# Performance work log

Measured on AMD Instinct MI355X. Metric: run time of the kernel, lower is better.

The kernel has to match this reference:

```python
import jax, jax.numpy as jnp
import numpy as np

HID = 768
NSPLITS = 12
HEAD_RATIO = 2
H = NSPLITS // HEAD_RATIO          # 6 attention heads
D = HID // NSPLITS                 # 64 head size
AH = H * D                         # 384 all_head_size
KS = 9                             # conv kernel size
PAD = (KS - 1) // 2
B, S = 4, 1024


def setup_inputs() -> dict:
    key = jax.random.key(0)
    ks = jax.random.split(key, 16)
    std = 0.02
    inp = {
        "Q": jax.random.normal(ks[0], (B, S, HID), jnp.float32),
        "K": jax.random.normal(ks[1], (B, S, HID), jnp.float32),
        "V": jax.random.normal(ks[2], (B, S, HID), jnp.float32),
        "td": jax.random.uniform(ks[3], (B, S), jnp.float32),
        "mask": jax.random.randint(ks[4], (B, S), 0, 2, jnp.int32),
        # projection weights, applied as x @ W (in, out)
        "Wq": jax.random.normal(ks[5], (HID, AH), jnp.float32) * std,
        "Wk": jax.random.normal(ks[6], (HID, AH), jnp.float32) * std,
        "Wv": jax.random.normal(ks[7], (HID, AH), jnp.float32) * std,
        # separable conv: depthwise (HID, KS), pointwise (AH, HID), bias (AH,)
        "dw_w": jax.random.normal(ks[8], (HID, KS), jnp.float32) * std,
        "pw_w": jax.random.normal(ks[9], (AH, HID), jnp.float32) * std,
        "sep_b": jnp.zeros((AH,), jnp.float32),
        # conv_kernel_layer Linear(AH -> H*KS)
        "ck_W": jax.random.normal(ks[10], (AH, H * KS), jnp.float32) * std,
        "ck_b": jnp.zeros((H * KS,), jnp.float32),
        # conv_out_layer Linear(HID -> AH)
        "co_W": jax.random.normal(ks[11], (HID, AH), jnp.float32) * std,
        "co_b": jnp.zeros((AH,), jnp.float32),
        # gammas init to zeros as in torch module
        "gammas": jnp.zeros((H, 1, 1), jnp.float32),
    }
    return inp


def dist_func(scores, td, am, gammas):
    # scores: [B,H,S,S]; am: [B,1,1,S] bool key mask; entirely non-differentiable.
    s = scores.shape[-1]
    dt = scores.dtype
    amf = am.astype(dt)
    p = jax.nn.softmax(jnp.where(am, scores, -1e8), axis=-1) * amf
    distcum = jnp.cumsum(p, axis=-1)
    disttotal = jnp.sum(p, axis=-1, keepdims=True)
    # |j - i| position distance
    pos = jnp.abs(jnp.arange(s)[None, :] - jnp.arange(s)[:, None]).astype(dt)
    dist_scores = jnp.sqrt(jnp.clip((disttotal - distcum) * pos[None, None], 0.0, None))
    gamma = -jax.nn.softplus(gammas)[None]  # (1,H,1,1)
    total_effect = jnp.clip(jnp.exp(dist_scores * gamma), 1e-5, 1e5)
    # time-distance effect on strictly-lower-triangular positions
    tdn = td / jnp.maximum(jnp.linalg.norm(td, axis=-1, keepdims=True), 1e-12)
    td_scores = jnp.broadcast_to(tdn[:, None, None, :], scores.shape)
    td_sm = jax.nn.softmax(jnp.where(am, td_scores, -1e4), axis=-1)
    lower = jnp.tril(jnp.ones((s, s), dt), -1)  # (triu == 0)
    return jax.lax.stop_gradient(total_effect - td_sm * lower[None, None])


def reference(Q, K, V, td, mask, Wq, Wk, Wv, dw_w, pw_w, sep_b, ck_W, ck_b, co_W, co_b, gammas):
    b, s, hid = Q.shape
    mq = Q @ Wq  # (B,S,AH)
    mk = K @ Wk
    mv = V @ Wv
    # SeparableConv1D over sequence dim of K
    x = jnp.transpose(K, (0, 2, 1))  # (B,HID,S)
    dw = jax.lax.conv_general_dilated(
        x, dw_w[:, None, :], window_strides=(1,), padding=[(PAD, PAD)],
        feature_group_count=hid, dimension_numbers=("NCH", "OIH", "NCH"))
    pw = jnp.einsum("bcs,oc->bos", dw, pw_w) + sep_b[None, :, None]
    mkc = jnp.transpose(pw, (0, 2, 1))  # (B,S,AH)

    q = mq.reshape(b, s, H, D).transpose(0, 2, 1, 3)
    k = mk.reshape(b, s, H, D).transpose(0, 2, 1, 3)
    v = mv.reshape(b, s, H, D).transpose(0, 2, 1, 3)

    # dynamic span convolution
    conv_attn = mkc * mq                                   # (B,S,AH)
    ck = (conv_attn @ ck_W + ck_b).reshape(b, s, H, KS)
    ck = jax.nn.softmax(ck, axis=-1)                       # per-position kernel
    co = V @ co_W + co_b                                   # (B,S,AH)
    co_pad = jnp.pad(co, ((0, 0), (PAD, PAD), (0, 0)))
    idx = jnp.arange(s)[:, None] + jnp.arange(KS)[None, :]  # (S,KS)
    unf = co_pad[:, idx, :].reshape(b, s, KS, H, D)         # sliding window gather
    conv_out = jnp.einsum("bskhd,bshk->bshd", unf, ck)      # (B,S,H,D)

    # attention with distance decay
    scores = jnp.einsum("bhid,bhjd->bhij", q, k) / np.float32(np.sqrt(D))
    am = (mask[:, None, None, :] != 0)  # (B,1,1,S) key mask
    total_effect = dist_func(scores, td, am, gammas)
    scores = jnp.where(am, scores * total_effect, -1e8)
    probs = jax.nn.softmax(scores, axis=-1)
    ctx = jnp.einsum("bhij,bhjd->bhid", probs, v).transpose(0, 2, 1, 3)  # (B,S,H,D)

    out = jnp.concatenate([ctx, conv_out], axis=2).reshape(b, s, HEAD_RATIO * AH)
    return out
```

## Files before the change

kernel.cpp:

```cpp
#include <hip/hip_runtime.h>
#include <hip/hip_bf16.h>

#define HIDC 768
#define Hh   6
#define Dd   64
#define AHc  384
#define KSc  9
#define PADc 4
#define Bb   4
#define Ss   1024
#define MRr  (Bb * Ss)

typedef __attribute__((ext_vector_type(8))) __bf16 bf16x8;
typedef __attribute__((ext_vector_type(4))) __bf16 bf16x4;
typedef __attribute__((ext_vector_type(4))) float  f32x4;

__device__ __forceinline__ void gl_lds16(const void* g, void* l) {
    __builtin_amdgcn_global_load_lds(
        (const __attribute__((address_space(1))) void*)g,
        (__attribute__((address_space(3))) void*)l, 16, 0, 0);
}

__device__ __forceinline__ void split8(const float* p, bf16x8& hi, bf16x8& lo) {
    float4 x0 = *(const float4*)p;
    float4 x1 = *(const float4*)(p + 4);
    float xs[8] = {x0.x, x0.y, x0.z, x0.w, x1.x, x1.y, x1.z, x1.w};
#pragma unroll
    for (int e = 0; e < 8; ++e) {
        __bf16 hv = (__bf16)xs[e];
        hi[e] = hv;
        lo[e] = (__bf16)(xs[e] - (float)hv);
    }
}

__device__ __forceinline__ void split8r(const float* xs, bf16x8& hi, bf16x8& lo) {
#pragma unroll
    for (int e = 0; e < 8; ++e) {
        __bf16 hv = (__bf16)xs[e];
        hi[e] = hv;
        lo[e] = (__bf16)(xs[e] - (float)hv);
    }
}

__device__ __forceinline__ bf16x8 cvt8(const float* p) {
    float4 x0 = *(const float4*)p;
    float4 x1 = *(const float4*)(p + 4);
    float xs[8] = {x0.x, x0.y, x0.z, x0.w, x1.x, x1.y, x1.z, x1.w};
    bf16x8 h;
#pragma unroll
    for (int e = 0; e < 8; ++e) h[e] = (__bf16)xs[e];
    return h;
}

__global__ void k_dwab(const float* __restrict__ Kin, const float* __restrict__ dww,
                       const float* __restrict__ Q, const float* __restrict__ V,
                       __bf16* __restrict__ dwbf,
                       __bf16* __restrict__ qbf, __bf16* __restrict__ vbf) {
    int bid = blockIdx.x;
    if (bid < 3072) {
        int idx = bid * 256 + threadIdx.x;
        int c4 = idx % (HIDC / 4);
        int s  = (idx / (HIDC / 4)) % Ss;
        int b  = idx / ((HIDC / 4) * Ss);
        int c  = c4 * 4;
        float wv[4][KSc];
#pragma unroll
        for (int j = 0; j < 4; ++j)
#pragma unroll
            for (int k = 0; k < KSc; ++k) wv[j][k] = dww[(c + j) * KSc + k];
        float4 acc = {0.f, 0.f, 0.f, 0.f};
#pragma unroll
        for (int k = 0; k < KSc; ++k) {
            int sp = s + k - PADc;
            if (sp >= 0 && sp < Ss) {
                float4 v = *(const float4*)&Kin[(size_t)(b * Ss + sp) * HIDC + c];
                acc.x += v.x * wv[0][k]; acc.y += v.y * wv[1][k];
                acc.z += v.z * wv[2][k]; acc.w += v.w * wv[3][k];
            }
        }
        bf16x4 o = {(__bf16)acc.x, (__bf16)acc.y, (__bf16)acc.z, (__bf16)acc.w};
        *(bf16x4*)(dwbf + (size_t)idx * 4) = o;
    } else {
        const int n8 = MRr * HIDC / 8;
        int idx = (bid - 3072) * 256 + threadIdx.x;
        if (idx < n8) {
            *(bf16x8*)(qbf + (size_t)idx * 8) = cvt8(Q + (size_t)idx * 8);
        } else {
            int i = idx - n8;
            *(bf16x8*)(vbf + (size_t)i * 8) = cvt8(V + (size_t)i * 8);
        }
    }
}

__global__ __launch_bounds__(256) void k_wsplit_t(const float* __restrict__ Wq, const float* __restrict__ Wk,
                                                  const float* __restrict__ Wv, const float* __restrict__ coW,
                                                  __bf16* __restrict__ Whi, __bf16* __restrict__ Wlo) {
    int z = blockIdx.z;
    const float* src = (z == 0) ? Wq : (z == 1) ? Wk : (z == 2) ? Wv : coW;
    int n0 = blockIdx.x * 64, k0 = blockIdx.y * 64;
    int tid = threadIdx.x;
    int r = tid >> 2, cq = tid & 3;
    __shared__ float tile[64][65];
#pragma unroll
    for (int e = 0; e < 4; ++e) {
        float4 v = *(const float4*)&src[(size_t)(k0 + r) * AHc + n0 + cq * 16 + e * 4];
        tile[r][cq * 16 + e * 4 + 0] = v.x;
        tile[r][cq * 16 + e * 4 + 1] = v.y;
        tile[r][cq * 16 + e * 4 + 2] = v.z;
        tile[r][cq * 16 + e * 4 + 3] = v.w;
    }
    __syncthreads();
    float x[16];
#pragma unroll
    for (int e = 0; e < 16; ++e) x[e] = tile[cq * 16 + e][r];
    bf16x8 h0, l0, h1, l1;
    split8r(x, h0, l0);
    split8r(x + 8, h1, l1);
    size_t dst = ((size_t)(z * AHc + n0 + r)) * HIDC + k0 + cq * 16;
    *(bf16x8*)(Whi + dst)     = h0;
    *(bf16x8*)(Whi + dst + 8) = h1;
    *(bf16x8*)(Wlo + dst)     = l0;
    *(bf16x8*)(Wlo + dst + 8) = l1;
}

__global__ __launch_bounds__(256) void k_misc(const float* __restrict__ pww,
                                              const float* __restrict__ cob, const float* __restrict__ sepb,
                                              const float* __restrict__ td, const int* __restrict__ mask,
                                              __bf16* __restrict__ Whi, __bf16* __restrict__ Wlo,
                                              float* __restrict__ biasb, float* __restrict__ td_sm) {
    int bid = blockIdx.x;
    int tid = threadIdx.x;
    if (bid < 144) {
        int idx = bid * 256 + tid;
        bf16x8 hi, lo;
        split8(pww + (size_t)idx * 8, hi, lo);
        size_t dst = (size_t)4 * AHc * HIDC + (size_t)idx * 8;
        *(bf16x8*)(Whi + dst) = hi;
        *(bf16x8*)(Wlo + dst) = lo;
        return;
    }
    if (bid < 152) {
        int idx = (bid - 144) * 256 + tid;
        if (idx < 5 * AHc) {
            int z = idx / AHc, n = idx % AHc;
            biasb[idx] = (z == 3) ? cob[n] : (z == 4) ? sepb[n] : 0.f;
        }
        return;
    }
    int b = bid - 152;
    __shared__ float red[256];
    __shared__ float tv[Ss];
    float ls = 0.f;
    for (int j = tid; j < Ss; j += 256) {
        float v = td[b * Ss + j];
        tv[j] = v;
        ls += v * v;
    }
    red[tid] = ls; __syncthreads();
    for (int s = 128; s > 0; s >>= 1) { if (tid < s) red[tid] += red[tid + s]; __syncthreads(); }
    float norm = fmaxf(sqrtf(red[0]), 1e-12f);
    __syncthreads();
    float lm = -3e38f;
    for (int j = tid; j < Ss; j += 256) {
        float v = mask[b * Ss + j] ? tv[j] / norm : -1e4f;
        tv[j] = v;
        lm = fmaxf(lm, v);
    }
    red[tid] = lm; __syncthreads();
    for (int s = 128; s > 0; s >>= 1) { if (tid < s) red[tid] = fmaxf(red[tid], red[tid + s]); __syncthreads(); }
    float m = red[0]; __syncthreads();
    float lsum = 0.f;
    for (int j = tid; j < Ss; j += 256) {
        float e = expf(tv[j] - m);
        tv[j] = e;
        lsum += e;
    }
    red[tid] = lsum; __syncthreads();
    for (int s = 128; s > 0; s >>= 1) { if (tid < s) red[tid] += red[tid + s]; __syncthreads(); }
    float inv = 1.f / red[0];
    __syncthreads();
    for (int j = tid; j < Ss; j += 256)
        td_sm[b * Ss + j] = tv[j] * inv;
}

__global__ __launch_bounds__(256) void k_gemm5(
        const __bf16* __restrict__ qbf, const float* __restrict__ Kin,
        const __bf16* __restrict__ vbf, const __bf16* __restrict__ dwbf,
        const __bf16* __restrict__ Whi, const __bf16* __restrict__ Wlo,
        const float* __restrict__ biasb, float* __restrict__ Call,
        __bf16* __restrict__ kh, __bf16* __restrict__ kl,
        __bf16* __restrict__ qh, __bf16* __restrict__ vt) {
    __shared__ __attribute__((aligned(16))) __bf16 As [128 * 32];
    __shared__ __attribute__((aligned(16))) __bf16 BsH[128 * 32];
    __shared__ __attribute__((aligned(16))) __bf16 BsL[128 * 32];

    int wg = blockIdx.x + 3 * (blockIdx.y + 32 * blockIdx.z);
    int n2 = (wg & 7) * 60 + (wg >> 3);
    int bxx = n2 % 3, byy = (n2 / 3) % 32, z = n2 / 96;

    int m0 = byy * 128, n0 = bxx * 128;
    int tid = threadIdx.x;
    int wave = tid >> 6, lane = tid & 63, quad = lane >> 4, l15 = lane & 15;

    int lrow = lane >> 2;
    int lswz = 8 * ((lane & 3) ^ (lrow & 3));

    int brow = wave * 32 + lrow;
    const __bf16* BhG0 = Whi + ((size_t)(z * AHc + n0 + brow)) * HIDC + lswz;
    const __bf16* BhG1 = BhG0 + (size_t)16 * HIDC;
    const __bf16* BlG0 = Wlo + ((size_t)(z * AHc + n0 + brow)) * HIDC + lswz;
    const __bf16* BlG1 = BlG0 + (size_t)16 * HIDC;
    __bf16* BhL0 = BsH + (wave * 2 + 0) * 512;
    __bf16* BhL1 = BsH + (wave * 2 + 1) * 512;
    __bf16* BlL0 = BsL + (wave * 2 + 0) * 512;
    __bf16* BlL1 = BsL + (wave * 2 + 1) * 512;

    const __bf16* Abf = (z == 0) ? qbf : (z == 4) ? dwbf : vbf;
    const __bf16* AG0 = Abf + ((size_t)(m0 + wave * 32 + lrow)) * HIDC + lswz;
    const __bf16* AG1 = AG0 + (size_t)16 * HIDC;
    __bf16* AL0 = As + (wave * 2 + 0) * 512;
    __bf16* AL1 = As + (wave * 2 + 1) * 512;

    int sr = tid >> 1;
    int sk = (tid & 1) * 16;
    const float* Arow = Kin + (size_t)(m0 + sr) * HIDC + sk;
    int g0 = sk >> 3;
    int d0 = sr * 32 + ((g0       ^ (sr & 3)) * 8);
    int d1 = sr * 32 + (((g0 + 1) ^ (sr & 3)) * 8);

    int swz = (quad ^ (l15 & 3)) * 8;
    f32x4 acc[4][4] = {};

    for (int k0 = 0; k0 < HIDC; k0 += 32) {
        if (z == 1) {
            const float* ap = Arow + k0;
            *(bf16x8*)&As[d0] = cvt8(ap);
            *(bf16x8*)&As[d1] = cvt8(ap + 8);
        } else {
            gl_lds16(AG0 + k0, AL0);
            gl_lds16(AG1 + k0, AL1);
        }
        gl_lds16(BhG0 + k0, BhL0);
        gl_lds16(BhG1 + k0, BhL1);
        gl_lds16(BlG0 + k0, BlL0);
        gl_lds16(BlG1 + k0, BlL1);
        __syncthreads();

        int mrow = (wave >> 1) * 64 + l15;
        int nrow = (wave & 1) * 64 + l15;
        bf16x8 ah[4], bh[4], bl[4];
#pragma unroll
        for (int mt = 0; mt < 4; ++mt)
            ah[mt] = *(bf16x8*)&As[(mrow + mt * 16) * 32 + swz];
#pragma unroll
        for (int nt = 0; nt < 4; ++nt) {
            bh[nt] = *(bf16x8*)&BsH[(nrow + nt * 16) * 32 + swz];
            bl[nt] = *(bf16x8*)&BsL[(nrow + nt * 16) * 32 + swz];
        }
#pragma unroll
        for (int mt = 0; mt < 4; ++mt)
#pragma unroll
            for (int nt = 0; nt < 4; ++nt) {
                acc[mt][nt] = __builtin_amdgcn_mfma_f32_16x16x32_bf16(ah[mt], bh[nt], acc[mt][nt], 0, 0, 0);
                acc[mt][nt] = __builtin_amdgcn_mfma_f32_16x16x32_bf16(ah[mt], bl[nt], acc[mt][nt], 0, 0, 0);
            }
        __syncthreads();
    }

    if (z == 1) {
#pragma unroll
        for (int nt = 0; nt < 4; ++nt) {
            int n = n0 + (wave & 1) * 64 + nt * 16 + l15;
#pragma unroll
            for (int mt = 0; mt < 4; ++mt) {
#pragma unroll
                for (int r = 0; r < 4; ++r) {
                    int m = m0 + (wave >> 1) * 64 + mt * 16 + quad * 4 + r;
                    float v = acc[mt][nt][r];
                    __bf16 hv = (__bf16)v;
                    kh[(size_t)m * AHc + n] = hv;
                    kl[(size_t)m * AHc + n] = (__bf16)(v - (float)hv);
                }
            }
        }
    } else if (z == 2) {
        int b = m0 >> 10;
#pragma unroll
        for (int nt = 0; nt < 4; ++nt) {
            int n = (wave & 1) * 64 + nt * 16 + l15;
            int gn = n0 + n;
            int h = gn >> 6, d = gn & 63;
#pragma unroll
            for (int mt = 0; mt < 4; ++mt) {
                int m = m0 + (wave >> 1) * 64 + mt * 16 + quad * 4;
                int s = m & (Ss - 1);
                bf16x4 o = {(__bf16)acc[mt][nt][0], (__bf16)acc[mt][nt][1],
                            (__bf16)acc[mt][nt][2], (__bf16)acc[mt][nt][3]};
                *(bf16x4*)&vt[((size_t)((b * Hh + h) * Dd + d)) * Ss + s] = o;
            }
        }
    } else if (z == 0) {
#pragma unroll
        for (int nt = 0; nt < 4; ++nt) {
            int n = n0 + (wave & 1) * 64 + nt * 16 + l15;
#pragma unroll
            for (int mt = 0; mt < 4; ++mt) {
#pragma unroll
                for (int r = 0; r < 4; ++r) {
                    int m = m0 + (wave >> 1) * 64 + mt * 16 + quad * 4 + r;
                    float v = acc[mt][nt][r];
                    Call[(size_t)m * AHc + n] = v;
                    qh[(size_t)m * AHc + n] = (__bf16)v;
                }
            }
        }
    } else {
        float* Cz = Call + (size_t)z * MRr * AHc;
        const float* bz = biasb + z * AHc;
#pragma unroll
        for (int nt = 0; nt < 4; ++nt) {
            int n = n0 + (wave & 1) * 64 + nt * 16 + l15;
            float bias = bz[n];
#pragma unroll
            for (int mt = 0; mt < 4; ++mt) {
#pragma unroll
                for (int r = 0; r < 4; ++r) {
                    int m = m0 + (wave >> 1) * 64 + mt * 16 + quad * 4 + r;
                    Cz[(size_t)m * AHc + n] = acc[mt][nt][r] + bias;
                }
            }
        }
    }
}

__global__ __launch_bounds__(64) void k_ck(const float* __restrict__ mkc, const float* __restrict__ mq,
                                           const float* __restrict__ ckW, const float* __restrict__ ckb,
                                           float* __restrict__ ck_sm) {
    int row = blockIdx.x;
    int tid = threadIdx.x;
    __shared__ float ca[AHc];
    __shared__ float ckv[Hh * KSc];
    for (int o = tid; o < AHc; o += 64)
        ca[o] = mkc[row * AHc + o] * mq[row * AHc + o];
    __syncthreads();
    if (tid < Hh * KSc) {
        float acc = ckb[tid];
        for (int o = 0; o < AHc; ++o)
            acc += ca[o] * ckW[o * (Hh * KSc) + tid];
        ckv[tid] = acc;
    }
    __syncthreads();
    if (tid < Hh) {
        float m = -3e38f;
#pragma unroll
        for (int k = 0; k < KSc; ++k) m = fmaxf(m, ckv[tid * KSc + k]);
        float e[KSc];
        float s = 0.f;
#pragma unroll
        for (int k = 0; k < KSc; ++k) { e[k] = expf(ckv[tid * KSc + k] - m); s += e[k]; }
        float inv = 1.f / s;
#pragma unroll
        for (int k = 0; k < KSc; ++k) ck_sm[(row * Hh + tid) * KSc + k] = e[k] * inv;
    }
}

__global__ void k_convout(const float* __restrict__ co, const float* __restrict__ ck_sm,
                          float* __restrict__ out) {
    int idx = blockIdx.x * 256 + threadIdx.x;
    if (idx >= Bb * Ss * AHc / 4) return;
    int d4 = idx & 15;
    int h  = (idx >> 4) % Hh;
    int s  = (idx / (AHc / 4)) % Ss;
    int b  = idx / ((AHc / 4) * Ss);
    int row = b * Ss + s;
    const float* ck = ck_sm + (size_t)(row * Hh + h) * KSc;
    float4 acc = {0.f, 0.f, 0.f, 0.f};
#pragma unroll
    for (int k = 0; k < KSc; ++k) {
        int sp = s + k - PADc;
        if (sp >= 0 && sp < Ss) {
            float4 v = *(const float4*)&co[(size_t)(b * Ss + sp) * AHc + h * Dd + d4 * 4];
            float wv = ck[k];
            acc.x += wv * v.x; acc.y += wv * v.y; acc.z += wv * v.z; acc.w += wv * v.w;
        }
    }
    *(float4*)&out[(size_t)row * (2 * AHc) + AHc + h * Dd + d4 * 4] = acc;
}

__device__ __forceinline__ int scix(int m, int j) {
    return m * 1024 + (j ^ (((m ^ (j >> 6)) & 7) << 2));
}

__global__ __launch_bounds__(512) void k_attn(const __bf16* __restrict__ qh,
                                              const __bf16* __restrict__ kh, const __bf16* __restrict__ kl,
                                              const __bf16* __restrict__ vt,
                                              const int* __restrict__ mask,
                                              const float* __restrict__ td_sm, const float* __restrict__ gammas,
                                              float* __restrict__ out) {
    __shared__ float sc[16 * 1024];
    int wg = blockIdx.x + 64 * blockIdx.y;
    int n  = (wg & 7) * 192 + (wg >> 3);
    int bx = n & 63, by = n >> 6;
    int i0 = bx * 16;
    int h = by % Hh, b = by / Hh;
    int tid = threadIdx.x;
    int w = tid >> 6, lane = tid & 63, quad = lane >> 4, l15 = lane & 15;
    int jw = w * 128;

    bf16x8 a_hi[2];
    {
        size_t qoff = (size_t)(b * Ss + i0 + l15) * AHc + h * Dd + quad * 8;
        a_hi[0] = *(const bf16x8*)(qh + qoff);
        a_hi[1] = *(const bf16x8*)(qh + qoff + 32);
    }
#pragma unroll 2
    for (int t = 0; t < 8; ++t) {
        int jt = jw + t * 16;
        size_t koff = (size_t)(b * Ss + jt + l15) * AHc + h * Dd + quad * 8;
        f32x4 acc = {0.f, 0.f, 0.f, 0.f};
#pragma unroll
        for (int kc = 0; kc < 2; ++kc) {
            bf16x8 khv = *(const bf16x8*)(kh + koff + kc * 32);
            bf16x8 klv = *(const bf16x8*)(kl + koff + kc * 32);
            acc = __builtin_amdgcn_mfma_f32_16x16x32_bf16(a_hi[kc], khv, acc, 0, 0, 0);
            acc = __builtin_amdgcn_mfma_f32_16x16x32_bf16(a_hi[kc], klv, acc, 0, 0, 0);
        }
#pragma unroll
        for (int r = 0; r < 4; ++r)
            sc[scix(quad * 4 + r, jt + l15)] = acc[r] * 0.125f;
    }
    __syncthreads();

    const int* mrow = mask + b * Ss;
    const float* tdrow = td_sm + b * Ss;
    float gamma = -log1pf(expf(gammas[h]));
    int jb = lane << 4;
    __attribute__((aligned(16))) int marr[16];
    {
        const int4* mp = (const int4*)(mrow + jb);
#pragma unroll
        for (int k = 0; k < 4; ++k) ((int4*)marr)[k] = mp[k];
    }
    __attribute__((aligned(16))) float tdv[16];
    {
        const float4* tp = (const float4*)(tdrow + jb);
#pragma unroll
        for (int k = 0; k < 4; ++k) ((float4*)tdv)[k] = tp[k];
    }

#pragma unroll
    for (int r4 = 0; r4 < 2; ++r4) {
        int m = w * 2 + r4;
        int i = i0 + m;
        __attribute__((aligned(16))) float s[16];
        float p[16];
#pragma unroll
        for (int g = 0; g < 4; ++g)
            *(f32x4*)(s + 4 * g) = *(const f32x4*)&sc[scix(m, jb + 4 * g)];
        float mx = -1e30f;
#pragma unroll
        for (int jj = 0; jj < 16; ++jj) mx = fmaxf(mx, marr[jj] ? s[jj] : -1e30f);
        mx = fmaxf(mx, __shfl_xor(mx, 1));  mx = fmaxf(mx, __shfl_xor(mx, 2));
        mx = fmaxf(mx, __shfl_xor(mx, 4));  mx = fmaxf(mx, __shfl_xor(mx, 8));
        mx = fmaxf(mx, __shfl_xor(mx, 16)); mx = fmaxf(mx, __shfl_xor(mx, 32));
#pragma unroll
        for (int jj = 0; jj < 16; ++jj) p[jj] = marr[jj] ? __expf(s[jj] - mx) : 0.f;
#pragma unroll
        for (int jj = 1; jj < 16; ++jj) p[jj] += p[jj - 1];
        float t = p[15];
        float incl = t;
#pragma unroll
        for (int dlt = 1; dlt < 64; dlt <<= 1) {
            float v = __shfl_up(incl, dlt);
            if (lane >= dlt) incl += v;
        }
        float off = incl - t;
        float tot = __shfl(incl, 63);
        float inv = 1.f / fmaxf(tot, 1e-30f);
        float mx2 = -1e30f;
#pragma unroll
        for (int jj = 0; jj < 16; ++jj) {
            int j = jb + jj;
            float cum = p[jj] + off;
            float pos = fabsf((float)(j - i));
            float ds = sqrtf(fmaxf((tot - cum) * inv * pos, 0.f));
            float te = fminf(fmaxf(__expf(ds * gamma), 1e-5f), 1e5f);
            float mult = te - ((j < i) ? tdv[jj] : 0.f);
            float s2 = marr[jj] ? s[jj] * mult : -1e8f;
            s[jj] = s2;
            mx2 = fmaxf(mx2, s2);
        }
        mx2 = fmaxf(mx2, __shfl_xor(mx2, 1));  mx2 = fmaxf(mx2, __shfl_xor(mx2, 2));
        mx2 = fmaxf(mx2, __shfl_xor(mx2, 4));  mx2 = fmaxf(mx2, __shfl_xor(mx2, 8));
        mx2 = fmaxf(mx2, __shfl_xor(mx2, 16)); mx2 = fmaxf(mx2, __shfl_xor(mx2, 32));
        float sm = 0.f;
#pragma unroll
        for (int jj = 0; jj < 16; ++jj) { s[jj] = __expf(s[jj] - mx2); sm += s[jj]; }
        sm += __shfl_xor(sm, 1);  sm += __shfl_xor(sm, 2);
        sm += __shfl_xor(sm, 4);  sm += __shfl_xor(sm, 8);
        sm += __shfl_xor(sm, 16); sm += __shfl_xor(sm, 32);
        float inv2 = 1.f / sm;
#pragma unroll
        for (int jj = 0; jj < 16; ++jj) s[jj] *= inv2;
#pragma unroll
        for (int g = 0; g < 4; ++g)
            *(f32x4*)&sc[scix(m, jb + 4 * g)] = *(const f32x4*)(s + 4 * g);
    }
    __syncthreads();

    f32x4 oacc[4] = {};
    const __bf16* vtb = vt + (size_t)(b * Hh + h) * Dd * Ss;
#pragma unroll
    for (int kc = 0; kc < 4; ++kc) {
        int j0 = jw + kc * 32 + quad * 8;
        __attribute__((aligned(16))) float x[8];
        *(f32x4*)x       = *(const f32x4*)&sc[scix(l15, j0)];
        *(f32x4*)(x + 4) = *(const f32x4*)&sc[scix(l15, j0 + 4)];
        bf16x8 p_hi, p_lo;
        split8r(x, p_hi, p_lo);
#pragma unroll
        for (int nt = 0; nt < 4; ++nt) {
            int d = nt * 16 + l15;
            bf16x8 vv = *(const bf16x8*)(vtb + (size_t)d * Ss + j0);
            oacc[nt] = __builtin_amdgcn_mfma_f32_16x16x32_bf16(p_hi, vv, oacc[nt], 0, 0, 0);
            oacc[nt] = __builtin_amdgcn_mfma_f32_16x16x32_bf16(p_lo, vv, oacc[nt], 0, 0, 0);
        }
    }
    __syncthreads();
#pragma unroll
    for (int nt = 0; nt < 4; ++nt)
#pragma unroll
        for (int r = 0; r < 4; ++r)
            sc[w * 1024 + (quad * 4 + r) * 64 + nt * 16 + l15] = oacc[nt][r];
    __syncthreads();
#pragma unroll
    for (int e = 0; e < 2; ++e) {
        int idx = e * 512 + tid;
        int m = idx >> 6, dd = idx & 63;
        float v = 0.f;
#pragma unroll
        for (int ww = 0; ww < 8; ++ww) v += sc[ww * 1024 + idx];
        out[(size_t)(b * Ss + i0 + m) * (2 * AHc) + h * Dd + dd] = v;
    }
}

extern "C" void kernel_launch(void* const* d_in, const int* in_sizes, int n_in,
                              void* d_out, int out_size, void* d_ws, size_t ws_size,
                              hipStream_t stream) {
    const float* Q    = (const float*)d_in[0];
    const float* Kin  = (const float*)d_in[1];
    const float* V    = (const float*)d_in[2];
    const float* td   = (const float*)d_in[3];
    const int*   mask = (const int*)d_in[4];
    const float* Wq   = (const float*)d_in[5];
    const float* Wk   = (const float*)d_in[6];
    const float* Wv   = (const float*)d_in[7];
    const float* dww  = (const float*)d_in[8];
    const float* pww  = (const float*)d_in[9];
    const float* sepb = (const float*)d_in[10];
    const float* ckW  = (const float*)d_in[11];
    const float* ckb  = (const float*)d_in[12];
    const float* coW  = (const float*)d_in[13];
    const float* cob  = (const float*)d_in[14];
    const float* gam  = (const float*)d_in[15];
    float* out = (float*)d_out;
    float* ws = (float*)d_ws;

    float* mq    = ws;
    float* mks   = mq    + (size_t)MRr * AHc;
    float* mvs   = mks   + (size_t)MRr * AHc;
    float* co    = mvs   + (size_t)MRr * AHc;
    float* mkc   = co    + (size_t)MRr * AHc;
    float* dwr   = mkc   + (size_t)MRr * AHc;
    float* cksm  = dwr   + (size_t)MRr * HIDC;
    float* tdsm  = cksm  + (size_t)MRr * Hh * KSc;
    float* biasb = tdsm  + (size_t)Bb * Ss;

    __bf16* dwbf = (__bf16*)dwr;
    __bf16* qbf  = (__bf16*)(dwr + (size_t)MRr * HIDC / 2);
    __bf16* kh = (__bf16*)mks;
    __bf16* kl = kh + (size_t)MRr * AHc;
    __bf16* vt = (__bf16*)mvs;
    __bf16* qh = vt + (size_t)MRr * AHc;

    __bf16* Whi = (__bf16*)d_out;
    __bf16* Wlo = Whi + (size_t)5 * AHc * HIDC;
    __bf16* vbf = Wlo + (size_t)5 * AHc * HIDC;

    dim3 gt(AHc / 64, HIDC / 64, 4);
    k_wsplit_t<<<gt, 256, 0, stream>>>(Wq, Wk, Wv, coW, Whi, Wlo);
    k_misc<<<156, 256, 0, stream>>>(pww, cob, sepb, td, mask, Whi, Wlo, biasb, tdsm);
    k_dwab<<<6144, 256, 0, stream>>>(Kin, dww, Q, V, dwbf, qbf, vbf);

    dim3 gg(AHc / 128, MRr / 128, 5);
    k_gemm5<<<gg, 256, 0, stream>>>(qbf, Kin, vbf, dwbf, Whi, Wlo, biasb, mq, kh, kl, qh, vt);

    k_ck<<<MRr, 64, 0, stream>>>(mkc, mq, ckW, ckb, cksm);
    k_convout<<<(MRr * AHc / 4 + 255) / 256, 256, 0, stream>>>(co, cksm, out);

    dim3 ga(Ss / 16, Bb * Hh);
    k_attn<<<ga, 512, 0, stream>>>(qh, kh, kl, vt, mask, tdsm, gam, out);
}
```

Measured before the change: 281.7 us.

## Merge preprocessing kernels, fuse ck softmax with conv-out, interleave attention row pairs

Three preprocessing kernels (weight split/transpose, misc bias/td softmax, depthwise conv plus bf16 casts) are merged into one launch. The per-row kernel-weight softmax and the dynamic conv output are fused into one kernel that handles 4 rows per block, dropping the intermediate ck buffer and one launch. In attention, the two per-wave rows of the distance-decay softmax are processed interleaved for more ILP, the QK loop unroll is raised, and a min-blocks launch bound is added. Register pressure from the interleaving and the occupancy hint could cause spills.

```diff
diff --git a/kernel.cpp b/kernel.cpp
--- a/kernel.cpp
+++ b/kernel.cpp
@@ -52,13 +52,106 @@
     return h;
 }
 
-__global__ void k_dwab(const float* __restrict__ Kin, const float* __restrict__ dww,
-                       const float* __restrict__ Q, const float* __restrict__ V,
-                       __bf16* __restrict__ dwbf,
-                       __bf16* __restrict__ qbf, __bf16* __restrict__ vbf) {
+__global__ __launch_bounds__(256) void k_pre(
+        const float* __restrict__ Wq, const float* __restrict__ Wk,
+        const float* __restrict__ Wv, const float* __restrict__ coW,
+        const float* __restrict__ pww, const float* __restrict__ cob,
+        const float* __restrict__ sepb, const float* __restrict__ td,
+        const int* __restrict__ mask, const float* __restrict__ Kin,
+        const float* __restrict__ dww, const float* __restrict__ Q,
+        const float* __restrict__ V,
+        __bf16* __restrict__ Whi, __bf16* __restrict__ Wlo,
+        float* __restrict__ biasb, float* __restrict__ td_sm,
+        __bf16* __restrict__ dwbf, __bf16* __restrict__ qbf,
+        __bf16* __restrict__ vbf) {
+    __shared__ float shmem[64 * 65];
     int bid = blockIdx.x;
-    if (bid < 3072) {
-        int idx = bid * 256 + threadIdx.x;
+    int tid = threadIdx.x;
+    if (bid < 288) {
+        int z = bid / 72, rem = bid % 72;
+        int n0 = (rem % 6) * 64, k0 = (rem / 6) * 64;
+        const float* src = (z == 0) ? Wq : (z == 1) ? Wk : (z == 2) ? Wv : coW;
+        float (*tile)[65] = (float(*)[65])shmem;
+        int r = tid >> 2, cq = tid & 3;
+#pragma unroll
+        for (int e = 0; e < 4; ++e) {
+            float4 v = *(const float4*)&src[(size_t)(k0 + r) * AHc + n0 + cq * 16 + e * 4];
+            tile[r][cq * 16 + e * 4 + 0] = v.x;
+            tile[r][cq * 16 + e * 4 + 1] = v.y;
+            tile[r][cq * 16 + e * 4 + 2] = v.z;
+            tile[r][cq * 16 + e * 4 + 3] = v.w;
+        }
+        __syncthreads();
+        float x[16];
+#pragma unroll
+        for (int e = 0; e < 16; ++e) x[e] = tile[cq * 16 + e][r];
+        bf16x8 h0, l0, h1, l1;
+        split8r(x, h0, l0);
+        split8r(x + 8, h1, l1);
+        size_t dst = ((size_t)(z * AHc + n0 + r)) * HIDC + k0 + cq * 16;
+        *(bf16x8*)(Whi + dst)     = h0;
+        *(bf16x8*)(Whi + dst + 8) = h1;
+        *(bf16x8*)(Wlo + dst)     = l0;
+        *(bf16x8*)(Wlo + dst + 8) = l1;
+        return;
+    }
+    if (bid < 432) {
+        int idx = (bid - 288) * 256 + tid;
+        bf16x8 hi, lo;
+        split8(pww + (size_t)idx * 8, hi, lo);
+        size_t dst = (size_t)4 * AHc * HIDC + (size_t)idx * 8;
+        *(bf16x8*)(Whi + dst) = hi;
+        *(bf16x8*)(Wlo + dst) = lo;
+        return;
+    }
+    if (bid < 440) {
+        int idx = (bid - 432) * 256 + tid;
+        if (idx < 5 * AHc) {
+            int z = idx / AHc, n = idx % AHc;
+            biasb[idx] = (z == 3) ? cob[n] : (z == 4) ? sepb[n] : 0.f;
+        }
+        return;
+    }
+    if (bid < 444) {
+        int b = bid - 440;
+        float* red = shmem;
+        float* tv  = shmem + 256;
+        float ls = 0.f;
+        for (int j = tid; j < Ss; j += 256) {
+            float v = td[b * Ss + j];
+            tv[j] = v;
+            ls += v * v;
+        }
+        red[tid] = ls; __syncthreads();
+        for (int s = 128; s > 0; s >>= 1) { if (tid < s) red[tid] += red[tid + s]; __syncthreads(); }
+        float norm = fmaxf(sqrtf(red[0]), 1e-12f);
+        __syncthreads();
+        float lm = -3e38f;
+        for (int j = tid; j < Ss; j += 256) {
+            float v = mask[b * Ss + j] ? tv[j] / norm : -1e4f;
+            tv[j] = v;
+            lm = fmaxf(lm, v);
+        }
+        red[tid] = lm; __syncthreads();
+        for (int s = 128; s > 0; s >>= 1) { if (tid < s) red[tid] = fmaxf(red[tid], red[tid + s]); __syncthreads(); }
+        float m = red[0]; __syncthreads();
+        float lsum = 0.f;
+        for (int j = tid; j < Ss; j += 256) {
+            float e = expf(tv[j] - m);
+            tv[j] = e;
+            lsum += e;
+        }
+        red[tid] = lsum; __syncthreads();
+        for (int s = 128; s > 0; s >>= 1) { if (tid < s) red[tid] += red[tid + s]; __syncthreads(); }
+        float inv = 1.f / red[0];
+        __syncthreads();
+        for (int j = tid; j < Ss; j += 256)
+            td_sm[b * Ss + j] = tv[j] * inv;
+        return;
+    }
+    int db = bid - 444;
+    if (db < 3072) {
+        int idx = db * 256 + tid;
         int c4 = idx % (HIDC / 4);
         int s  = (idx / (HIDC / 4)) % Ss;
         int b  = idx / ((HIDC / 4) * Ss);
@@ -82,7 +175,7 @@
         *(bf16x4*)(dwbf + (size_t)idx * 4) = o;
     } else {
         const int n8 = MRr * HIDC / 8;
-        int idx = (bid - 3072) * 256 + threadIdx.x;
+        int idx = (db - 3072) * 256 + tid;
         if (idx < n8) {
             *(bf16x8*)(qbf + (size_t)idx * 8) = cvt8(Q + (size_t)idx * 8);
         } else {
@@ -90,97 +183,6 @@
             *(bf16x8*)(vbf + (size_t)i * 8) = cvt8(V + (size_t)i * 8);
         }
     }
-}
-
-__global__ __launch_bounds__(256) void k_wsplit_t(const float* __restrict__ Wq, const float* __restrict__ Wk,
-                                                  const float* __restrict__ Wv, const float* __restrict__ coW,
-                                                  __bf16* __restrict__ Whi, __bf16* __restrict__ Wlo) {
-    int z = blockIdx.z;
-    const float* src = (z == 0) ? Wq : (z == 1) ? Wk : (z == 2) ? Wv : coW;
-    int n0 = blockIdx.x * 64, k0 = blockIdx.y * 64;
-    int tid = threadIdx.x;
-    int r = tid >> 2, cq = tid & 3;
-    __shared__ float tile[64][65];
-#pragma unroll
-    for (int e = 0; e < 4; ++e) {
-        float4 v = *(const float4*)&src[(size_t)(k0 + r) * AHc + n0 + cq * 16 + e * 4];
-        tile[r][cq * 16 + e * 4 + 0] = v.x;
-        tile[r][cq * 16 + e * 4 + 1] = v.y;
-        tile[r][cq * 16 + e * 4 + 2] = v.z;
-        tile[r][cq * 16 + e * 4 + 3] = v.w;
-    }
-    __syncthreads();
-    float x[16];
-#pragma unroll
-    for (int e = 0; e < 16; ++e) x[e] = tile[cq * 16 + e][r];
-    bf16x8 h0, l0, h1, l1;
-    split8r(x, h0, l0);
-    split8r(x + 8, h1, l1);
-    size_t dst = ((size_t)(z * AHc + n0 + r)) * HIDC + k0 + cq * 16;
-    *(bf16x8*)(Whi + dst)     = h0;
-    *(bf16x8*)(Whi + dst + 8) = h1;
-    *(bf16x8*)(Wlo + dst)     = l0;
-    *(bf16x8*)(Wlo + dst + 8) = l1;
-}
-
-__global__ __launch_bounds__(256) void k_misc(const float* __restrict__ pww,
-                                              const float* __restrict__ cob, const float* __restrict__ sepb,
-                                              const float* __restrict__ td, const int* __restrict__ mask,
-                                              __bf16* __restrict__ Whi, __bf16* __restrict__ Wlo,
-                                              float* __restrict__ biasb, float* __restrict__ td_sm) {
-    int bid = blockIdx.x;
-    int tid = threadIdx.x;
-    if (bid < 144) {
-        int idx = bid * 256 + tid;
-        bf16x8 hi, lo;
-        split8(pww + (size_t)idx * 8, hi, lo);
-        size_t dst = (size_t)4 * AHc * HIDC + (size_t)idx * 8;
-        *(bf16x8*)(Whi + dst) = hi;
-        *(bf16x8*)(Wlo + dst) = lo;
-        return;
-    }
-    if (bid < 152) {
-        int idx = (bid - 144) * 256 + tid;
-        if (idx < 5 * AHc) {
-            int z = idx / AHc, n = idx % AHc;
-            biasb[idx] = (z == 3) ? cob[n] : (z == 4) ? sepb[n] : 0.f;
-        }
-        return;
-    }
-    int b = bid - 152;
-    __shared__ float red[256];
-    __shared__ float tv[Ss];
-    float ls = 0.f;
-    for (int j = tid; j < Ss; j += 256) {
-        float v = td[b * Ss + j];
-        tv[j] = v;
-        ls += v * v;
-    }
-    red[tid] = ls; __syncthreads();
-    for (int s = 128; s > 0; s >>= 1) { if (tid < s) red[tid] += red[tid + s]; __syncthreads(); }
-    float norm = fmaxf(sqrtf(red[0]), 1e-12f);
-    __syncthreads();
-    float lm = -3e38f;
-    for (int j = tid; j < Ss; j += 256) {
-        float v = mask[b * Ss + j] ? tv[j] / norm : -1e4f;
-        tv[j] = v;
-        lm = fmaxf(lm, v);
-    }
-    red[tid] = lm; __syncthreads();
-    for (int s = 128; s > 0; s >>= 1) { if (tid < s) red[tid] = fmaxf(red[tid], red[tid + s]); __syncthreads(); }
-    float m = red[0]; __syncthreads();
-    float lsum = 0.f;
-    for (int j = tid; j < Ss; j += 256) {
-        float e = expf(tv[j] - m);
-        tv[j] = e;
-        lsum += e;
-    }
-    red[tid] = lsum; __syncthreads();
-    for (int s = 128; s > 0; s >>= 1) { if (tid < s) red[tid] += red[tid + s]; __syncthreads(); }
-    float inv = 1.f / red[0];
-    __syncthreads();
-    for (int j = tid; j < Ss; j += 256)
-        td_sm[b * Ss + j] = tv[j] * inv;
 }
 
 __global__ __launch_bounds__(256) void k_gemm5(
@@ -333,65 +335,67 @@
     }
 }
 
-__global__ __launch_bounds__(64) void k_ck(const float* __restrict__ mkc, const float* __restrict__ mq,
-                                           const float* __restrict__ ckW, const float* __restrict__ ckb,
-                                           float* __restrict__ ck_sm) {
-    int row = blockIdx.x;
+__global__ __launch_bounds__(256) void k_ckconv(const float* __restrict__ mkc,
+                                                const float* __restrict__ mq,
+                                                const float* __restrict__ ckW,
+                                                const float* __restrict__ ckb,
+                                                const float* __restrict__ co,
+                                                float* __restrict__ out) {
     int tid = threadIdx.x;
-    __shared__ float ca[AHc];
-    __shared__ float ckv[Hh * KSc];
-    for (int o = tid; o < AHc; o += 64)
-        ca[o] = mkc[row * AHc + o] * mq[row * AHc + o];
+    int lr = tid >> 6, lane = tid & 63;
+    int row = blockIdx.x * 4 + lr;
+    __shared__ float ca[4][AHc];
+    __shared__ float ckv[4][Hh * KSc];
+    for (int o = lane; o < AHc; o += 64)
+        ca[lr][o] = mkc[(size_t)row * AHc + o] * mq[(size_t)row * AHc + o];
     __syncthreads();
-    if (tid < Hh * KSc) {
-        float acc = ckb[tid];
+    if (lane < Hh * KSc) {
+        float acc = ckb[lane];
         for (int o = 0; o < AHc; ++o)
-            acc += ca[o] * ckW[o * (Hh * KSc) + tid];
-        ckv[tid] = acc;
+            acc += ca[lr][o] * ckW[o * (Hh * KSc) + lane];
+        ckv[lr][lane] = acc;
     }
     __syncthreads();
-    if (tid < Hh) {
+    if (lane < Hh) {
         float m = -3e38f;
 #pragma unroll
-        for (int k = 0; k < KSc; ++k) m = fmaxf(m, ckv[tid * KSc + k]);
+        for (int k = 0; k < KSc; ++k) m = fmaxf(m, ckv[lr][lane * KSc + k]);
         float e[KSc];
         float s = 0.f;
 #pragma unroll
-        for (int k = 0; k < KSc; ++k) { e[k] = expf(ckv[tid * KSc + k] - m); s += e[k]; }
+        for (int k = 0; k < KSc; ++k) { e[k] = expf(ckv[lr][lane * KSc + k] - m); s += e[k]; }
         float inv = 1.f / s;
 #pragma unroll
-        for (int k = 0; k < KSc; ++k) ck_sm[(row * Hh + tid) * KSc + k] = e[k] * inv;
-    }
-}
-
-__global__ void k_convout(const float* __restrict__ co, const float* __restrict__ ck_sm,
-                          float* __restrict__ out) {
-    int idx = blockIdx.x * 256 + threadIdx.x;
-    if (idx >= Bb * Ss * AHc / 4) return;
-    int d4 = idx & 15;
-    int h  = (idx >> 4) % Hh;
-    int s  = (idx / (AHc / 4)) % Ss;
-    int b  = idx / ((AHc / 4) * Ss);
-    int row = b * Ss + s;
-    const float* ck = ck_sm + (size_t)(row * Hh + h) * KSc;
-    float4 acc = {0.f, 0.f, 0.f, 0.f};
-#pragma unroll
-    for (int k = 0; k < KSc; ++k) {
-        int sp = s + k - PADc;
-        if (sp >= 0 && sp < Ss) {
-            float4 v = *(const float4*)&co[(size_t)(b * Ss + sp) * AHc + h * Dd + d4 * 4];
-            float wv = ck[k];
-            acc.x += wv * v.x; acc.y += wv * v.y; acc.z += wv * v.z; acc.w += wv * v.w;
-        }
-    }
-    *(float4*)&out[(size_t)row * (2 * AHc) + AHc + h * Dd + d4 * 4] = acc;
+        for (int k = 0; k < KSc; ++k) ckv[lr][lane * KSc + k] = e[k] * inv;
+    }
+    __syncthreads();
+#pragma unroll
+    for (int e = 0; e < 2; ++e) {
+        int it = e * 256 + tid;
+        if (it >= 4 * (AHc / 4)) break;
+        int r4i = it / (AHc / 4), dq = it % (AHc / 4);
+        int h = dq >> 4, d4 = dq & 15;
+        int row2 = blockIdx.x * 4 + r4i;
+        int s = row2 & (Ss - 1), b = row2 >> 10;
+        float4 acc = {0.f, 0.f, 0.f, 0.f};
+#pragma unroll
+        for (int k = 0; k < KSc; ++k) {
+            int sp = s + k - PADc;
+            if (sp >= 0 && sp < Ss) {
+                float4 v = *(const float4*)&co[(size_t)(b * Ss + sp) * AHc + h * Dd + d4 * 4];
+                float wv = ckv[r4i][h * KSc + k];
+                acc.x += wv * v.x; acc.y += wv * v.y; acc.z += wv * v.z; acc.w += wv * v.w;
+            }
+        }
+        *(float4*)&out[(size_t)row2 * (2 * AHc) + AHc + h * Dd + d4 * 4] = acc;
+    }
 }
 
 __device__ __forceinline__ int scix(int m, int j) {
     return m * 1024 + (j ^ (((m ^ (j >> 6)) & 7) << 2));
 }
 
-__global__ __launch_bounds__(512) void k_attn(const __bf16* __restrict__ qh,
+__global__ __launch_bounds__(512, 4) void k_attn(const __bf16* __restrict__ qh,
                                               const __bf16* __restrict__ kh, const __bf16* __restrict__ kl,
                                               const __bf16* __restrict__ vt,
                                               const int* __restrict__ mask,
@@ -413,7 +417,7 @@
         a_hi[0] = *(const bf16x8*)(qh + qoff);
         a_hi[1] = *(const bf16x8*)(qh + qoff + 32);
     }
-#pragma unroll 2
+#pragma unroll 4
     for (int t = 0; t < 8; ++t) {
         int jt = jw + t * 16;
         size_t koff = (size_t)(b * Ss + jt + l15) * AHc + h * Dd + quad * 8;
@@ -448,63 +452,88 @@
         for (int k = 0; k < 4; ++k) ((float4*)tdv)[k] = tp[k];
     }
 
-#pragma unroll
-    for (int r4 = 0; r4 < 2; ++r4) {
-        int m = w * 2 + r4;
-        int i = i0 + m;
-        __attribute__((aligned(16))) float s[16];
-        float p[16];
-#pragma unroll
-        for (int g = 0; g < 4; ++g)
-            *(f32x4*)(s + 4 * g) = *(const f32x4*)&sc[scix(m, jb + 4 * g)];
-        float mx = -1e30f;
-#pragma unroll
-        for (int jj = 0; jj < 16; ++jj) mx = fmaxf(mx, marr[jj] ? s[jj] : -1e30f);
-        mx = fmaxf(mx, __shfl_xor(mx, 1));  mx = fmaxf(mx, __shfl_xor(mx, 2));
-        mx = fmaxf(mx, __shfl_xor(mx, 4));  mx = fmaxf(mx, __shfl_xor(mx, 8));
-        mx = fmaxf(mx, __shfl_xor(mx, 16)); mx = fmaxf(mx, __shfl_xor(mx, 32));
-#pragma unroll
-        for (int jj = 0; jj < 16; ++jj) p[jj] = marr[jj] ? __expf(s[jj] - mx) : 0.f;
-#pragma unroll
-        for (int jj = 1; jj < 16; ++jj) p[jj] += p[jj - 1];
-        float t = p[15];
-        float incl = t;
+    {
+        int mA = w * 2, mB = mA + 1;
+        int iA = i0 + mA, iB = i0 + mB;
+        __attribute__((aligned(16))) float sA[16], sB[16];
+        float pA[16], pB[16];
+#pragma unroll
+        for (int g = 0; g < 4; ++g) {
+            *(f32x4*)(sA + 4 * g) = *(const f32x4*)&sc[scix(mA, jb + 4 * g)];
+            *(f32x4*)(sB + 4 * g) = *(const f32x4*)&sc[scix(mB, jb + 4 * g)];
+        }
+        float mxA = -1e30f, mxB = -1e30f;
+#pragma unroll
+        for (int jj = 0; jj < 16; ++jj) {
+            mxA = fmaxf(mxA, marr[jj] ? sA[jj] : -1e30f);
+            mxB = fmaxf(mxB, marr[jj] ? sB[jj] : -1e30f);
+        }
+#pragma unroll
+        for (int d = 1; d < 64; d <<= 1) {
+            mxA = fmaxf(mxA, __shfl_xor(mxA, d));
+            mxB = fmaxf(mxB, __shfl_xor(mxB, d));
+        }
+#pragma unroll
+        for (int jj = 0; jj < 16; ++jj) {
+            pA[jj] = marr[jj] ? __expf(sA[jj] - mxA) : 0.f;
+            pB[jj] = marr[jj] ? __expf(sB[jj] - mxB) : 0.f;
+        }
+#pragma unroll
+        for (int jj = 1; jj < 16; ++jj) { pA[jj] += pA[jj - 1]; pB[jj] += pB[jj - 1]; }
+        float tA = pA[15], tB = pB[15];
+        float incA = tA, incB = tB;
 #pragma unroll
         for (int dlt = 1; dlt < 64; dlt <<= 1) {
-            float v = __shfl_up(incl, dlt);
-            if (lane >= dlt) incl += v;
-        }
-        float off = incl - t;
-        float tot = __shfl(incl, 63);
-        float inv = 1.f / fmaxf(tot, 1e-30f);
-        float mx2 = -1e30f;
+            float vA = __shfl_up(incA, dlt);
+            float vB = __shfl_up(incB, dlt);
+            if (lane >= dlt) { incA += vA; incB += vB; }
+        }
+        float offA = incA - tA, offB = incB - tB;
+        float totA = __shfl(incA, 63), totB = __shfl(incB, 63);
+        float invA = 1.f / fmaxf(totA, 1e-30f), invB = 1.f / fmaxf(totB, 1e-30f);
+        float mx2A = -1e30f, mx2B = -1e30f;
 #pragma unroll
         for (int jj = 0; jj < 16; ++jj) {
             int j = jb + jj;
-            float cum = p[jj] + off;
-            float pos = fabsf((float)(j - i));
-            float ds = sqrtf(fmaxf((tot - cum) * inv * pos, 0.f));
-            float te = fminf(fmaxf(__expf(ds * gamma), 1e-5f), 1e5f);
-            float mult = te - ((j < i) ? tdv[jj] : 0.f);
-            float s2 = marr[jj] ? s[jj] * mult : -1e8f;
-            s[jj] = s2;
-            mx2 = fmaxf(mx2, s2);
-        }
-        mx2 = fmaxf(mx2, __shfl_xor(mx2, 1));  mx2 = fmaxf(mx2, __shfl_xor(mx2, 2));
-        mx2 = fmaxf(mx2, __shfl_xor(mx2, 4));  mx2 = fmaxf(mx2, __shfl_xor(mx2, 8));
-        mx2 = fmaxf(mx2, __shfl_xor(mx2, 16)); mx2 = fmaxf(mx2, __shfl_xor(mx2, 32));
-        float sm = 0.f;
-#pragma unroll
-        for (int jj = 0; jj < 16; ++jj) { s[jj] = __expf(s[jj] - mx2); sm += s[jj]; }
-        sm += __shfl_xor(sm, 1);  sm += __shfl_xor(sm, 2);
-        sm += __shfl_xor(sm, 4);  sm += __shfl_xor(sm, 8);
-        sm += __shfl_xor(sm, 16); sm += __shfl_xor(sm, 32);
-        float inv2 = 1.f / sm;
-#pragma unroll
-        for (int jj = 0; jj < 16; ++jj) s[jj] *= inv2;
-#pragma unroll
-        for (int g = 0; g < 4; ++g)
-            *(f32x4*)&sc[scix(m, jb + 4 * g)] = *(const f32x4*)(s + 4 * g);
+            float cumA = pA[jj] + offA, cumB = pB[jj] + offB;
+            float posA = fabsf((float)(j - iA));
+            float posB = fabsf((float)(j - iB));
+            float dsA = sqrtf(fmaxf((totA - cumA) * invA * posA, 0.f));
+            float dsB = sqrtf(fmaxf((totB - cumB) * invB * posB, 0.f));
+            float teA = fminf(fmaxf(__expf(dsA * gamma), 1e-5f), 1e5f);
+            float teB = fminf(fmaxf(__expf(dsB * gamma), 1e-5f), 1e5f);
+            float tdj = tdv[jj];
+            float multA = teA - ((j < iA) ? tdj : 0.f);
+            float multB = teB - ((j < iB) ? tdj : 0.f);
+            float s2A = marr[jj] ? sA[jj] * multA : -1e8f;
+            float s2B = marr[jj] ? sB[jj] * multB : -1e8f;
+            sA[jj] = s2A; sB[jj] = s2B;
+            mx2A = fmaxf(mx2A, s2A); mx2B = fmaxf(mx2B, s2B);
+        }
+#pragma unroll
+        for (int d = 1; d < 64; d <<= 1) {
+            mx2A = fmaxf(mx2A, __shfl_xor(mx2A, d));
+            mx2B = fmaxf(mx2B, __shfl_xor(mx2B, d));
+        }
+        float smA = 0.f, smB = 0.f;
+#pragma unroll
+        for (int jj = 0; jj < 16; ++jj) {
+            sA[jj] = __expf(sA[jj] - mx2A); smA += sA[jj];
+            sB[jj] = __expf(sB[jj] - mx2B); smB += sB[jj];
+        }
+#pragma unroll
+        for (int d = 1; d < 64; d <<= 1) {
+            smA += __shfl_xor(smA, d);
+            smB += __shfl_xor(smB, d);
+        }
+        float i2A = 1.f / smA, i2B = 1.f / smB;
+#pragma unroll
+        for (int jj = 0; jj < 16; ++jj) { sA[jj] *= i2A; sB[jj] *= i2B; }
+#pragma unroll
+        for (int g = 0; g < 4; ++g) {
+            *(f32x4*)&sc[scix(mA, jb + 4 * g)] = *(const f32x4*)(sA + 4 * g);
+            *(f32x4*)&sc[scix(mB, jb + 4 * g)] = *(const f32x4*)(sB + 4 * g);
+        }
     }
     __syncthreads();
 
@@ -572,8 +601,7 @@
     float* co    = mvs   + (size_t)MRr * AHc;
     float* mkc   = co    + (size_t)MRr * AHc;
     float* dwr   = mkc   + (size_t)MRr * AHc;
-    float* cksm  = dwr   + (size_t)MRr * HIDC;
-    float* tdsm  = cksm  + (size_t)MRr * Hh * KSc;
+    float* tdsm  = dwr   + (size_t)MRr * HIDC;
     float* biasb = tdsm  + (size_t)Bb * Ss;
 
     __bf16* dwbf = (__bf16*)dwr;
@@ -587,16 +615,14 @@
     __bf16* Wlo = Whi + (size_t)5 * AHc * HIDC;
     __bf16* vbf = Wlo + (size_t)5 * AHc * HIDC;
 
-    dim3 gt(AHc / 64, HIDC / 64, 4);
-    k_wsplit_t<<<gt, 256, 0, stream>>>(Wq, Wk, Wv, coW, Whi, Wlo);
-    k_misc<<<156, 256, 0, stream>>>(pww, cob, sepb, td, mask, Whi, Wlo, biasb, tdsm);
-    k_dwab<<<6144, 256, 0, stream>>>(Kin, dww, Q, V, dwbf, qbf, vbf);
+    k_pre<<<6588, 256, 0, stream>>>(Wq, Wk, Wv, coW, pww, cob, sepb, td, mask,
+                                    Kin, dww, Q, V, Whi, Wlo, biasb, tdsm,
+                                    dwbf, qbf, vbf);
 
     dim3 gg(AHc / 128, MRr / 128, 5);
     k_gemm5<<<gg, 256, 0, stream>>>(qbf, Kin, vbf, dwbf, Whi, Wlo, biasb, mq, kh, kl, qh, vt);
 
-    k_ck<<<MRr, 64, 0, stream>>>(mkc, mq, ckW, ckb, cksm);
-    k_convout<<<(MRr * AHc / 4 + 255) / 256, 256, 0, stream>>>(co, cksm, out);
+    k_ckconv<<<MRr / 4, 256, 0, stream>>>(mkc, mq, ckW, ckb, co, out);
 
     dim3 ga(Ss / 16, Bb * Hh);
     k_attn<<<ga, 512, 0, stream>>>(qh, kh, kl, vt, mask, tdsm, gam, out);
```

Result: faster. 272.6 us (-3.2%).
